# Kernel tuning notes

Hardware: AMD Instinct MI355X
Metric: run time of the kernel (lower is better)

The kernel has to match this reference:

```python
import jax, jax.numpy as jnp
import numpy as np

ENTITY_TYPES = ['PER', 'ORG', 'LOC', 'MISC', 'GPE', 'DATE', 'TIME', 'MONEY', 'PERCENT',
                'FAC', 'EVENT', 'LAW', 'LANGUAGE', 'NORP', 'ORDINAL', 'CARDINAL', 'PRODUCT', 'QUANTITY']
TAGS = ['<PAD>', 'O'] + [f'{p}-{t}' for t in ENTITY_TYPES for p in ('B', 'I')]
TAG2IDX = {t: i for i, t in enumerate(TAGS)}
PAD_IDX = TAG2IDX['<PAD>']
O_IDX = TAG2IDX['O']
LAMBDA_MISS = 1.2
LAMBDA_FP = 1.0
LAMBDA_TRANSITION = 0.8
EPS = 1e-8


def _split_tag(tag):
    if tag in {'O', '<PAD>'} or '-' not in tag:
        return (tag, None)
    prefix, label = tag.split('-', 1)
    return (prefix, label)


def build_valid_transition_mask():
    n = len(TAGS)
    valid = np.zeros((n, n), dtype=np.float32)
    for prev_idx, prev_tag in enumerate(TAGS):
        prev_prefix, prev_label = _split_tag(prev_tag)
        for curr_idx, curr_tag in enumerate(TAGS):
            curr_prefix, curr_label = _split_tag(curr_tag)
            if curr_tag == '<PAD>' or curr_tag == 'O' or curr_prefix == 'B':
                ok = True
            elif curr_prefix == 'I':
                ok = (prev_prefix in {'B', 'I'}) and (prev_label == curr_label)
            else:
                ok = False
            valid[prev_idx, curr_idx] = 1.0 if ok else 0.0
    return valid


def setup_inputs() -> dict:
    key = jax.random.key(0)
    k1, k2 = jax.random.split(key)
    B, T, C = 128, 4096, len(TAGS)  # C = 38
    logits = jax.random.normal(k1, (B, T, C), dtype=jnp.float32)
    labels = jax.random.randint(k2, (B, T), 0, C, dtype=jnp.int32)
    valid_transition_mask = jnp.asarray(build_valid_transition_mask())  # [C, C]
    return {'logits': logits, 'labels': labels, 'valid_transition_mask': valid_transition_mask}


def _masked_mean(x, mask):
    # mean of x over positions where mask is True (0 if mask empty)
    cnt = jnp.sum(mask)
    return jnp.sum(jnp.where(mask, x, 0.0)) / jnp.maximum(cnt, 1).astype(x.dtype)


def reference(logits, labels, valid_transition_mask):
    # logits: [B, T, C]; labels: [B, T] int; valid_transition_mask: [C, C]
    logp = jax.nn.log_softmax(logits, axis=-1)            # [B, T, C]
    probs = jnp.exp(logp)                                  # softmax(logits)

    valid = labels != PAD_IDX                              # [B, T]
    # cross entropy with ignore_index=PAD (unweighted mean over valid tokens)
    gold_logp = jnp.take_along_axis(logp, labels[..., None], axis=-1)[..., 0]
    ce_loss = _masked_mean(-gold_logp, valid)

    p_o = probs[..., O_IDX]                                # [B, T]
    gold_entity = valid & (labels != O_IDX)
    gold_o = valid & (labels == O_IDX)

    # miss penalty: -log(1 - p_o) on gold entity tokens
    miss_penalty = _masked_mean(-jnp.log(jnp.clip(1.0 - p_o, EPS)), gold_entity)
    # false-positive penalty: -log(1 - (1 - p_o)) = -log(p_o) on gold O tokens
    fp_penalty = _masked_mean(-jnp.log(jnp.clip(p_o, EPS)), gold_o)

    # transition penalty: sum of prev_probs (outer) curr_probs over invalid (prev,curr)
    # pairs. Algebraically: prev . (invalid @ curr) per position, avoids [B,T,C,C].
    invalid = 1.0 - valid_transition_mask                  # [C, C]
    invalid_mass = jnp.einsum('btc,cd,btd->bt', probs[:, :-1, :], invalid, probs[:, 1:, :])
    tmask = valid[:, 1:] & valid[:, :-1]
    transition_penalty = _masked_mean(invalid_mass, tmask)

    return (ce_loss + LAMBDA_MISS * miss_penalty + LAMBDA_FP * fp_penalty
            + LAMBDA_TRANSITION * transition_penalty)
```

## Files before the change

kernel.cpp:

```cpp
#include <hip/hip_runtime.h>


#define NCLS 38
#define SLICEF 2472

__global__ __launch_bounds__(256, 4) void ner_main(const float* __restrict__ logits,
                                                   const int* __restrict__ labels,
                                                   float* __restrict__ partials) {
    __shared__ float S[4][SLICEF];
    __shared__ float red[4][8];

    const int tid  = threadIdx.x;
    const int lane = tid & 63;
    const int wv   = tid >> 6;
    const int W    = blockIdx.x * 4 + wv;
    const long long tok0 = (long long)W * 64;
    const long long tok  = tok0 + lane;
    const bool tile_rowend = ((W & 63) == 63);
    const bool rowend = tile_rowend && (lane == 63);

    float* sl = S[wv];

    const int l     = labels[tok];
    const int lnext = labels[tok + (rowend ? 0 : 1)];
    {
        const float4* g4 = reinterpret_cast<const float4*>(logits + tok0 * NCLS);
#pragma unroll
        for (int i = 0; i < 10; ++i) {
            const int idx = lane + i * 64;
            if (idx < 608)
                __builtin_amdgcn_global_load_lds(
                    (const __attribute__((address_space(1))) void*)(g4 + idx),
                    (__attribute__((address_space(3))) void*)(sl + i * 256),
                    16, 0, 0);
        }
        if (!tile_rowend && lane < 10) {
            const float4* b4 = reinterpret_cast<const float4*>(logits + (tok0 + 64) * NCLS);
            __builtin_amdgcn_global_load_lds(
                (const __attribute__((address_space(1))) void*)(b4 + lane),
                (__attribute__((address_space(3))) void*)(sl + 2432),
                16, 0, 0);
        }
    }
    asm volatile("s_waitcnt vmcnt(0)" ::: "memory");

    float v[NCLS];
    {
        const float2* lp = reinterpret_cast<const float2*>(sl + lane * NCLS);
        float2* vv = reinterpret_cast<float2*>(v);
#pragma unroll
        for (int i = 0; i < NCLS / 2; ++i) vv[i] = lp[i];
    }
    const float gold = sl[lane * NCLS + l];

    float s = 0.f;
#pragma unroll
    for (int c = 0; c < NCLS; ++c) { const float e = __expf(v[c]); v[c] = e; s += e; }
    const float inv = 1.f / s;
    const float lg  = __logf(s);

    float ce_s = 0.f, mi_s = 0.f, fp_s = 0.f, tr_s = 0.f;
    float ce_c = 0.f, mi_c = 0.f, fp_c = 0.f, tr_c = 0.f;

    if (l != 0) {
        ce_s = lg - gold; ce_c = 1.f;
        const float po = v[1] * inv;
        if (l == 1) { fp_s = -__logf(fmaxf(po,       1e-8f)); fp_c = 1.f; }
        else        { mi_s = -__logf(fmaxf(1.f - po, 1e-8f)); mi_c = 1.f; }
    }

    float qv[18];
#pragma unroll
    for (int j = 0; j < 18; ++j) qv[j] = __shfl_down(v[3 + 2 * j], 1, 64);
    float qinv = __shfl_down(inv, 1, 64);

    if (!tile_rowend) {
        const float e0 = (lane < NCLS) ? __expf(sl[2432 + lane]) : 0.f;
        float bs = e0;
#pragma unroll
        for (int m = 32; m >= 1; m >>= 1) bs += __shfl_xor(bs, m, 64);
        float qb[18];
#pragma unroll
        for (int j = 0; j < 18; ++j) qb[j] = __shfl(e0, 3 + 2 * j, 64);
        if (lane == 63) {
#pragma unroll
            for (int j = 0; j < 18; ++j) qv[j] = qb[j];
            qinv = 1.f / bs;
        }
    }

    if (!rowend && l != 0 && lnext != 0) {
        float m = 0.f;
#pragma unroll
        for (int j = 0; j < 18; ++j)
            m += qv[j] * (s - v[2 + 2 * j] - v[3 + 2 * j]);
        tr_s = m * inv * qinv; tr_c = 1.f;
    }

    float vals[8] = {ce_s, mi_s, fp_s, tr_s, ce_c, mi_c, fp_c, tr_c};
#pragma unroll
    for (int k = 0; k < 8; ++k) {
        float x = vals[k];
#pragma unroll
        for (int off = 32; off >= 1; off >>= 1) x += __shfl_down(x, off, 64);
        vals[k] = x;
    }
    if (lane == 0) {
#pragma unroll
        for (int k = 0; k < 8; ++k) red[wv][k] = vals[k];
    }
    __syncthreads();
    if (tid < 8) {
        const float t = red[0][tid] + red[1][tid] + red[2][tid] + red[3][tid];
        partials[blockIdx.x * 8 + tid] = t;
    }
}

__global__ __launch_bounds__(1024) void ner_reduce(const float* __restrict__ partials,
                                                   float* __restrict__ out, int nblk) {
    __shared__ float acc[8];
    const int tid = threadIdx.x;
    if (tid < 8) acc[tid] = 0.f;
    __syncthreads();
    float s = 0.f;
    const int n = nblk * 8;
    for (int i = tid; i < n; i += 1024) s += partials[i];
    atomicAdd(&acc[tid & 7], s);
    __syncthreads();
    if (tid == 0) {
        const float ce = acc[0] / fmaxf(acc[4], 1.f);
        const float mi = acc[1] / fmaxf(acc[5], 1.f);
        const float fp = acc[2] / fmaxf(acc[6], 1.f);
        const float tr = acc[3] / fmaxf(acc[7], 1.f);
        out[0] = ce + 1.2f * mi + 1.0f * fp + 0.8f * tr;
    }
}

extern "C" void kernel_launch(void* const* d_in, const int* in_sizes, int n_in,
                              void* d_out, int out_size, void* d_ws, size_t ws_size,
                              hipStream_t stream) {
    const float* logits = (const float*)d_in[0];
    const int*   labels = (const int*)d_in[1];
    float* partials = (float*)d_ws;

    const long long N = (long long)in_sizes[1];
    const int nblk = (int)(N / 256);

    hipLaunchKernelGGL(ner_main, dim3(nblk), dim3(256), 0, stream, logits, labels, partials);
    hipLaunchKernelGGL(ner_reduce, dim3(1), dim3(1024), 0, stream, partials, (float*)d_out, nblk);
}
```

Before: 116.6 us.

## Use overlapping 64-token wave tiles with stride 63 instead of halo loads

Each wave now covers 63 new tokens plus one overlapping token, so the next-token softmax for the transition term comes from a lane shuffle. This removes the separate halo load and its block reduction and broadcast. Block-level LDS reduction and the barrier are dropped; each wave writes its partials directly, with the three counts packed into one float and decoded in the reduce kernel. The cost is an unaligned base that needs an extra float4 load, about 1.6% more waves doing redundant loads, and packed counts that rely on float precision within each wave.

```diff
diff --git a/kernel.cpp b/kernel.cpp
--- a/kernel.cpp
+++ b/kernel.cpp
@@ -2,47 +2,42 @@
 
 
 #define NCLS 38
-#define SLICEF 2472
+#define SLF 2440
 
 __global__ __launch_bounds__(256, 4) void ner_main(const float* __restrict__ logits,
                                                    const int* __restrict__ labels,
                                                    float* __restrict__ partials) {
-    __shared__ float S[4][SLICEF];
-    __shared__ float red[4][8];
+    __shared__ float S[4][SLF];
 
     const int tid  = threadIdx.x;
     const int lane = tid & 63;
     const int wv   = tid >> 6;
     const int W    = blockIdx.x * 4 + wv;
-    const long long tok0 = (long long)W * 64;
+    const int row  = (int)(((unsigned)W * 64528u) >> 22);
+    const int wrow = W - row * 65;
+    const long long tok0 = (long long)row * 4096 + 63 * wrow;
     const long long tok  = tok0 + lane;
-    const bool tile_rowend = ((W & 63) == 63);
-    const bool rowend = tile_rowend && (lane == 63);
 
     float* sl = S[wv];
 
-    const int l     = labels[tok];
-    const int lnext = labels[tok + (rowend ? 0 : 1)];
+    const int l = labels[tok];
     {
-        const float4* g4 = reinterpret_cast<const float4*>(logits + tok0 * NCLS);
+        const long long basef = tok0 * NCLS;
+        const int off = (int)(basef & 3);
+        const float4* g4 = reinterpret_cast<const float4*>(logits + (basef - off));
+        const int nf4 = 608 + (off ? 1 : 0);
 #pragma unroll
         for (int i = 0; i < 10; ++i) {
             const int idx = lane + i * 64;
-            if (idx < 608)
+            if (idx < nf4)
                 __builtin_amdgcn_global_load_lds(
                     (const __attribute__((address_space(1))) void*)(g4 + idx),
                     (__attribute__((address_space(3))) void*)(sl + i * 256),
                     16, 0, 0);
         }
-        if (!tile_rowend && lane < 10) {
-            const float4* b4 = reinterpret_cast<const float4*>(logits + (tok0 + 64) * NCLS);
-            __builtin_amdgcn_global_load_lds(
-                (const __attribute__((address_space(1))) void*)(b4 + lane),
-                (__attribute__((address_space(3))) void*)(sl + 2432),
-                16, 0, 0);
-        }
+        asm volatile("s_waitcnt vmcnt(0)" ::: "memory");
+        sl += off;
     }
-    asm volatile("s_waitcnt vmcnt(0)" ::: "memory");
 
     float v[NCLS];
     {
@@ -59,79 +54,78 @@
     const float inv = 1.f / s;
     const float lg  = __logf(s);
 
-    float ce_s = 0.f, mi_s = 0.f, fp_s = 0.f, tr_s = 0.f;
-    float ce_c = 0.f, mi_c = 0.f, fp_c = 0.f, tr_c = 0.f;
+    float ce_s = 0.f, mi_s = 0.f, fp_s = 0.f, tr_s = 0.f, cnt = 0.f;
 
-    if (l != 0) {
-        ce_s = lg - gold; ce_c = 1.f;
+    const bool own_tok = (lane < 63) || (wrow == 64);
+    if (own_tok && l != 0) {
+        ce_s = lg - gold; cnt += 1.f;
         const float po = v[1] * inv;
-        if (l == 1) { fp_s = -__logf(fmaxf(po,       1e-8f)); fp_c = 1.f; }
-        else        { mi_s = -__logf(fmaxf(1.f - po, 1e-8f)); mi_c = 1.f; }
+        if (l == 1) { fp_s = -__logf(fmaxf(po,       1e-8f)); cnt += 256.f; }
+        else        { mi_s = -__logf(fmaxf(1.f - po, 1e-8f)); }
     }
 
+    const int   lnext = __shfl_down(l, 1, 64);
+    const float qinv  = __shfl_down(inv, 1, 64);
     float qv[18];
 #pragma unroll
     for (int j = 0; j < 18; ++j) qv[j] = __shfl_down(v[3 + 2 * j], 1, 64);
-    float qinv = __shfl_down(inv, 1, 64);
 
-    if (!tile_rowend) {
-        const float e0 = (lane < NCLS) ? __expf(sl[2432 + lane]) : 0.f;
-        float bs = e0;
-#pragma unroll
-        for (int m = 32; m >= 1; m >>= 1) bs += __shfl_xor(bs, m, 64);
-        float qb[18];
-#pragma unroll
-        for (int j = 0; j < 18; ++j) qb[j] = __shfl(e0, 3 + 2 * j, 64);
-        if (lane == 63) {
-#pragma unroll
-            for (int j = 0; j < 18; ++j) qv[j] = qb[j];
-            qinv = 1.f / bs;
-        }
-    }
-
-    if (!rowend && l != 0 && lnext != 0) {
+    if (lane < 63 && l != 0 && lnext != 0) {
         float m = 0.f;
 #pragma unroll
         for (int j = 0; j < 18; ++j)
             m += qv[j] * (s - v[2 + 2 * j] - v[3 + 2 * j]);
-        tr_s = m * inv * qinv; tr_c = 1.f;
+        tr_s = m * inv * qinv; cnt += 65536.f;
     }
 
-    float vals[8] = {ce_s, mi_s, fp_s, tr_s, ce_c, mi_c, fp_c, tr_c};
+    float vals[5] = {ce_s, mi_s, fp_s, tr_s, cnt};
 #pragma unroll
-    for (int k = 0; k < 8; ++k) {
+    for (int k = 0; k < 5; ++k) {
         float x = vals[k];
 #pragma unroll
-        for (int off = 32; off >= 1; off >>= 1) x += __shfl_down(x, off, 64);
+        for (int o = 32; o >= 1; o >>= 1) x += __shfl_down(x, o, 64);
         vals[k] = x;
     }
     if (lane == 0) {
-#pragma unroll
-        for (int k = 0; k < 8; ++k) red[wv][k] = vals[k];
-    }
-    __syncthreads();
-    if (tid < 8) {
-        const float t = red[0][tid] + red[1][tid] + red[2][tid] + red[3][tid];
-        partials[blockIdx.x * 8 + tid] = t;
+        *reinterpret_cast<float4*>(partials + W * 8) =
+            make_float4(vals[0], vals[1], vals[2], vals[3]);
+        partials[W * 8 + 4] = vals[4];
     }
 }
 
 __global__ __launch_bounds__(1024) void ner_reduce(const float* __restrict__ partials,
-                                                   float* __restrict__ out, int nblk) {
-    __shared__ float acc[8];
+                                                   float* __restrict__ out, int nwaves) {
+    __shared__ float acc[7];
     const int tid = threadIdx.x;
-    if (tid < 8) acc[tid] = 0.f;
+    if (tid < 7) acc[tid] = 0.f;
     __syncthreads();
-    float s = 0.f;
-    const int n = nblk * 8;
-    for (int i = tid; i < n; i += 1024) s += partials[i];
-    atomicAdd(&acc[tid & 7], s);
+    float s_ce = 0.f, s_mi = 0.f, s_fp = 0.f, s_tr = 0.f;
+    float c_ce = 0.f, c_fp = 0.f, c_tr = 0.f;
+    for (int i = tid; i < nwaves; i += 1024) {
+        const float4 p = *reinterpret_cast<const float4*>(partials + i * 8);
+        const float pc = partials[i * 8 + 4];
+        s_ce += p.x; s_mi += p.y; s_fp += p.z; s_tr += p.w;
+        const float tc = floorf(pc * (1.f / 65536.f));
+        const float rem = pc - tc * 65536.f;
+        const float fc = floorf(rem * (1.f / 256.f));
+        c_tr += tc; c_fp += fc; c_ce += rem - fc * 256.f;
+    }
+    float vals[7] = {s_ce, s_mi, s_fp, s_tr, c_ce, c_fp, c_tr};
+#pragma unroll
+    for (int k = 0; k < 7; ++k) {
+        float x = vals[k];
+#pragma unroll
+        for (int o = 32; o >= 1; o >>= 1) x += __shfl_down(x, o, 64);
+        if ((tid & 63) == 0) atomicAdd(&acc[k], x);
+    }
     __syncthreads();
     if (tid == 0) {
-        const float ce = acc[0] / fmaxf(acc[4], 1.f);
-        const float mi = acc[1] / fmaxf(acc[5], 1.f);
-        const float fp = acc[2] / fmaxf(acc[6], 1.f);
-        const float tr = acc[3] / fmaxf(acc[7], 1.f);
+        const float ce_c = acc[4], fp_c = acc[5], tr_c = acc[6];
+        const float mi_c = ce_c - fp_c;
+        const float ce = acc[0] / fmaxf(ce_c, 1.f);
+        const float mi = acc[1] / fmaxf(mi_c, 1.f);
+        const float fp = acc[2] / fmaxf(fp_c, 1.f);
+        const float tr = acc[3] / fmaxf(tr_c, 1.f);
         out[0] = ce + 1.2f * mi + 1.0f * fp + 0.8f * tr;
     }
 }
@@ -144,8 +138,10 @@
     float* partials = (float*)d_ws;
 
     const long long N = (long long)in_sizes[1];
-    const int nblk = (int)(N / 256);
+    const int rows   = (int)(N / 4096);
+    const int nwaves = rows * 65;
+    const int nblk   = nwaves / 4;
 
     hipLaunchKernelGGL(ner_main, dim3(nblk), dim3(256), 0, stream, logits, labels, partials);
-    hipLaunchKernelGGL(ner_reduce, dim3(1), dim3(1024), 0, stream, partials, (float*)d_out, nblk);
+    hipLaunchKernelGGL(ner_reduce, dim3(1), dim3(1024), 0, stream, partials, (float*)d_out, nwaves);
 }
```

Result: no change. 117.8 us (+1.0%).
